# Optimization experiments

Measured on AMD Instinct MI355X. Metric: run time of the kernel, lower is better.

The kernel has to match this reference:

```python
import jax, jax.numpy as jnp
import numpy as np

CHANNELS = 32


def _mlp(x, W1, b1, W2, b2, W3, b3):
    # FNN: Linear -> ReLU -> Linear -> ReLU -> Linear (last layer linear)
    h = jax.nn.relu(x @ W1 + b1)
    h = jax.nn.relu(h @ W2 + b2)
    return h @ W3 + b3


def setup_inputs() -> dict:
    key = jax.random.key(0)
    ks = jax.random.split(key, 8)
    E = 262144
    C = CHANNELS
    H = 128
    d_in = 4  # 2 * spatial_dim
    d_out = C * (C + 1)  # 1056
    s = lambda fan_in: 1.0 / np.sqrt(fan_in)
    return {
        "pos_i": jax.random.normal(ks[0], (E, 2), jnp.float32),
        "pos_j": jax.random.normal(ks[1], (E, 2), jnp.float32),
        "v_j": jax.random.normal(ks[2], (E, C), jnp.float32),
        "W1": jax.random.normal(ks[3], (d_in, H), jnp.float32) * s(d_in),
        "b1": jnp.zeros((H,), jnp.float32),
        "W2": jax.random.normal(ks[4], (H, H), jnp.float32) * s(H),
        "b2": jnp.zeros((H,), jnp.float32),
        "W3": jax.random.normal(ks[5], (H, d_out), jnp.float32) * s(H),
        "b3": jnp.zeros((d_out,), jnp.float32),
    }


def reference(pos_i, pos_j, v_j, W1, b1, W2, b2, W3, b3):
    C = CHANNELS
    pos_ij = jnp.concatenate((pos_i, pos_j), axis=-1)          # [E, 2*spatial_dim]
    kernel = _mlp(pos_ij, W1, b1, W2, b2, W3, b3)
    kernel = kernel.reshape(-1, C, C + 1)                      # [E, C, C+1]
    mat, bias = kernel[..., :, :-1], kernel[..., :, -1]        # [E,C,C], [E,C]
    return jnp.einsum('eij,ej->ei', mat, v_j) + bias           # [E, C]
```

## Files before the change

### kernel.cpp

```cpp
#include <hip/hip_runtime.h>


#define E_TOTAL 262144
#define EPB 256
#define NBLK (E_TOTAL / EPB)

typedef float f32x4 __attribute__((ext_vector_type(4)));
typedef short s8v  __attribute__((ext_vector_type(8)));

__device__ __forceinline__ unsigned short f2bf(float x) {
  unsigned u = __float_as_uint(x);
  u += 0x7fffu + ((u >> 16) & 1u);
  return (unsigned short)(u >> 16);
}

__device__ __forceinline__ void gld16(const void* g, void* l) {
  __builtin_amdgcn_global_load_lds(
      (const __attribute__((address_space(1))) unsigned int*)g,
      (__attribute__((address_space(3))) unsigned int*)l, 16, 0, 0);
}

__global__ void prep_pack(const float* __restrict__ W2, const float* __restrict__ W3,
                          const float* __restrict__ b3,
                          unsigned short* __restrict__ Wg2, unsigned short* __restrict__ W2f,
                          unsigned short* __restrict__ b3f, float* __restrict__ b3c) {
  int idx = blockIdx.x * 256 + threadIdx.x;
  if (idx < 135168) {
    int jj = idx & 7, lane = (idx >> 3) & 63;
    int ksnn = idx >> 9, ks = ksnn & 3, nn = ksnn >> 2;
    int nnt = (nn < 33) ? (2 * nn) : (2 * (nn - 33) + 1);
    int k = ks * 32 + ((lane >> 4) << 3) + jj;
    int col = nnt * 16 + (lane & 15);
    int i = col & 31, j = col >> 5;
    Wg2[idx] = f2bf(W3[k * 1056 + i * 33 + j]);
  }
  if (idx < 16384) {
    int ks = idx >> 12, nt = (idx >> 9) & 7, l = (idx >> 3) & 63, jj = idx & 7;
    int k = ks * 32 + ((l >> 4) << 3) + jj;
    int n = nt * 16 + (l & 15);
    W2f[idx] = f2bf(W2[k * 128 + n]);
  }
  if (idx < 1024) {
    int jj = idx & 7, lane = (idx >> 3) & 63, ih = idx >> 9;
    int j = ((lane >> 4) << 3) + jj, i = ih * 16 + (lane & 15);
    b3f[idx] = f2bf(b3[i * 33 + j]);
  }
  if (idx < 32) b3c[idx] = b3[idx * 33 + 32];
}

template <int IH>
__device__ __forceinline__ void g_chunk(const unsigned short* __restrict__ buf,
                                        const float* __restrict__ vt,
                                        int j0, int lane, int eoff,
                                        const s8v (&af)[4][4], float (&oa)[2][4][4]) {
  const f32x4 zero4 = {0.f, 0.f, 0.f, 0.f};
#pragma unroll
  for (int t = 0; t < 3; ++t) {
    s8v bfr[4];
#pragma unroll
    for (int ks = 0; ks < 4; ++ks)
      bfr[ks] = *(const s8v*)&buf[t * 2048 + ks * 512 + lane * 8];
    f32x4 p[4];
#pragma unroll
    for (int m = 0; m < 4; ++m)
      p[m] = __builtin_amdgcn_mfma_f32_16x16x32_bf16(af[m][0], bfr[0], zero4, 0, 0, 0);
#pragma unroll
    for (int ks = 1; ks < 4; ++ks)
#pragma unroll
      for (int m = 0; m < 4; ++m)
        p[m] = __builtin_amdgcn_mfma_f32_16x16x32_bf16(af[m][ks], bfr[ks], p[m], 0, 0, 0);
    const float* vp = vt + (j0 + t) * 256 + eoff;
#pragma unroll
    for (int m = 0; m < 4; ++m) {
      f32x4 vv = *(const f32x4*)(vp + m * 16);
#pragma unroll
      for (int r = 0; r < 4; ++r) oa[IH][m][r] += vv[r] * p[m][r];
    }
  }
}

__global__ __launch_bounds__(256, 2) void fnn_fused(
    const float* __restrict__ pos_i, const float* __restrict__ pos_j,
    const float* __restrict__ vj, const float* __restrict__ W1,
    const float* __restrict__ b1, const float* __restrict__ b2,
    const unsigned short* __restrict__ W2f, const unsigned short* __restrict__ Wg2,
    const unsigned short* __restrict__ b3f, const float* __restrict__ b3c,
    float* __restrict__ out) {
  __shared__ __attribute__((aligned(16))) char smem[58368];
  float* vt = (float*)smem;
  unsigned short* Bb  = (unsigned short*)(smem + 33792);
  unsigned short* h1c = (unsigned short*)smem;
  unsigned short* h2n = (unsigned short*)(smem + 18432);

  const int tid = threadIdx.x;
  const int w = tid >> 6, lane = tid & 63, q = lane >> 4, ln = lane & 15;
  const int B0 = blockIdx.x * EPB;
  const int eoff = w * 64 + q * 4;

  float oa[2][4][4];
  {
    s8v av[4];
#pragma unroll
    for (int m = 0; m < 4; ++m) {
      int e = B0 + w * 64 + m * 16 + ln;
      const float4 va = *(const float4*)(vj + (size_t)e * 32 + q * 8);
      const float4 vb = *(const float4*)(vj + (size_t)e * 32 + q * 8 + 4);
      s8v t;
      t[0] = (short)f2bf(va.x); t[1] = (short)f2bf(va.y);
      t[2] = (short)f2bf(va.z); t[3] = (short)f2bf(va.w);
      t[4] = (short)f2bf(vb.x); t[5] = (short)f2bf(vb.y);
      t[6] = (short)f2bf(vb.z); t[7] = (short)f2bf(vb.w);
      av[m] = t;
    }
#pragma unroll
    for (int ih = 0; ih < 2; ++ih) {
      s8v b3fr = *(const s8v*)(b3f + (ih * 64 + lane) * 8);
      float cbv = b3c[ih * 16 + ln];
      f32x4 ci = {cbv, cbv, cbv, cbv};
#pragma unroll
      for (int m = 0; m < 4; ++m) {
        f32x4 p = __builtin_amdgcn_mfma_f32_16x16x32_bf16(av[m], b3fr, ci, 0, 0, 0);
#pragma unroll
        for (int r = 0; r < 4; ++r) oa[ih][m][r] = p[r];
      }
    }
  }

  const int hh0 = (tid & 15) * 8;
  float w1r[4][8], b1r[8], b2r[8];
#pragma unroll
  for (int d = 0; d < 4; ++d)
#pragma unroll
    for (int u = 0; u < 8; ++u) w1r[d][u] = W1[d * 128 + hh0 + u];
#pragma unroll
  for (int u = 0; u < 8; ++u) b1r[u] = b1[hh0 + u];
#pragma unroll
  for (int nt = 0; nt < 8; ++nt) b2r[nt] = b2[nt * 16 + ln];

  s8v af[4][4];
  for (int qtr = 0; qtr < 4; ++qtr) {
#pragma unroll
    for (int half = 0; half < 4; ++half) {
      int ee = (tid >> 4) + half * 16;
      int eg = B0 + qtr * 64 + ee;
      float2 pi = *(const float2*)(pos_i + (size_t)eg * 2);
      float2 pj = *(const float2*)(pos_j + (size_t)eg * 2);
      s8v hv;
#pragma unroll
      for (int u = 0; u < 8; ++u) {
        float o = b1r[u] + pi.x * w1r[0][u] + pi.y * w1r[1][u] +
                  pj.x * w1r[2][u] + pj.y * w1r[3][u];
        hv[u] = (short)f2bf(fmaxf(o, 0.f));
      }
      *(s8v*)&h1c[ee * 144 + hh0] = hv;
    }
    __syncthreads();
    {
      s8v afr[4];
#pragma unroll
      for (int ks = 0; ks < 4; ++ks)
        afr[ks] = *(const s8v*)&h1c[(w * 16 + ln) * 144 + ks * 32 + q * 8];
#pragma unroll
      for (int nt = 0; nt < 8; ++nt) {
        f32x4 a4 = {0.f, 0.f, 0.f, 0.f};
#pragma unroll
        for (int ks = 0; ks < 4; ++ks) {
          s8v bfr2 = *(const s8v*)(W2f + ((ks * 8 + nt) * 64 + lane) * 8);
          a4 = __builtin_amdgcn_mfma_f32_16x16x32_bf16(afr[ks], bfr2, a4, 0, 0, 0);
        }
#pragma unroll
        for (int r = 0; r < 4; ++r)
          h2n[(w * 16 + q * 4 + r) * 144 + nt * 16 + ln] =
              f2bf(fmaxf(a4[r] + b2r[nt], 0.f));
      }
    }
    __syncthreads();
    if (w == qtr) {
#pragma unroll
      for (int m = 0; m < 4; ++m)
#pragma unroll
        for (int ks = 0; ks < 4; ++ks)
          af[m][ks] = *(const s8v*)&h2n[(m * 16 + ln) * 144 + ks * 32 + q * 8];
    }
  }
  __syncthreads();

  {
    const float* vrow = vj + (size_t)(B0 + tid) * 32;
#pragma unroll
    for (int j4 = 0; j4 < 8; ++j4) {
      float4 vv = *(const float4*)(vrow + j4 * 4);
      vt[(j4 * 4 + 0) * 256 + tid] = vv.x;
      vt[(j4 * 4 + 1) * 256 + tid] = vv.y;
      vt[(j4 * 4 + 2) * 256 + tid] = vv.z;
      vt[(j4 * 4 + 3) * 256 + tid] = vv.w;
    }
    vt[32 * 256 + tid] = 1.0f;
  }

  {
    const char* g = (const char*)Wg2 + tid * 16;
    char* l = (char*)Bb + (tid & 192) * 16;
#pragma unroll
    for (int t = 0; t < 3; ++t) gld16(g + t * 4096, l + t * 4096);
  }
  __syncthreads();

  for (int c = 0; c < 22; ++c) {
    const unsigned short* buf = Bb + (c & 1) * 6144;
    if (c + 1 < 22) {
      const char* g = (const char*)Wg2 + (c + 1) * 12288 + tid * 16;
      char* l = (char*)Bb + ((c + 1) & 1) * 12288 + (tid & 192) * 16;
#pragma unroll
      for (int t = 0; t < 3; ++t) gld16(g + t * 4096, l + t * 4096);
    }
    if (c < 11) g_chunk<0>(buf, vt, c * 3, lane, eoff, af, oa);
    else        g_chunk<1>(buf, vt, (c - 11) * 3, lane, eoff, af, oa);
    __syncthreads();
  }

#pragma unroll
  for (int m = 0; m < 4; ++m)
#pragma unroll
    for (int ih = 0; ih < 2; ++ih)
#pragma unroll
      for (int r = 0; r < 4; ++r) {
        int e = B0 + w * 64 + m * 16 + q * 4 + r;
        out[(size_t)e * 32 + ih * 16 + ln] = oa[ih][m][r];
      }
}

extern "C" void kernel_launch(void* const* d_in, const int* in_sizes, int n_in,
                              void* d_out, int out_size, void* d_ws, size_t ws_size,
                              hipStream_t stream) {
  const float* pos_i = (const float*)d_in[0];
  const float* pos_j = (const float*)d_in[1];
  const float* vj    = (const float*)d_in[2];
  const float* W1    = (const float*)d_in[3];
  const float* b1    = (const float*)d_in[4];
  const float* W2    = (const float*)d_in[5];
  const float* b2    = (const float*)d_in[6];
  const float* W3    = (const float*)d_in[7];
  const float* b3    = (const float*)d_in[8];
  float* outp = (float*)d_out;

  unsigned short* Wg2 = (unsigned short*)d_ws;
  unsigned short* W2f = (unsigned short*)((char*)d_ws + 270336);
  unsigned short* b3f = (unsigned short*)((char*)d_ws + 303104);
  float*          b3c = (float*)((char*)d_ws + 305152);

  prep_pack<<<528, 256, 0, stream>>>(W2, W3, b3, Wg2, W2f, b3f, b3c);
  fnn_fused<<<NBLK, 256, 0, stream>>>(pos_i, pos_j, vj, W1, b1, b2, W2f, Wg2, b3f, b3c, outp);
}
```

Before: 218.9 us.

## Double edges per block to 512 and store v transpose as bf16 in LDS

Each block now handles 512 edges with 512 threads, so every W3 chunk staged in LDS is reused by twice as many edges and the per-block global-to-LDS weight traffic is amortized. The transposed v buffer is kept in bf16 to fit the larger tile in LDS, and the layer-1/2 row padding shrinks from 144 to 136. The B-fragment loads are interleaved with the MFMAs, and b2 is loaded per tile instead of held in registers to cut register pressure. In exchange, occupancy demands rise (launch bounds 512 threads with 4 blocks requested, about 68KB LDS per block), and v is rounded to bf16 in the final contraction, which lowers precision.

```diff
diff --git a/kernel.cpp b/kernel.cpp
--- a/kernel.cpp
+++ b/kernel.cpp
@@ -2,7 +2,7 @@
 
 
 #define E_TOTAL 262144
-#define EPB 256
+#define EPB 512
 #define NBLK (E_TOTAL / EPB)
 
 typedef float f32x4 __attribute__((ext_vector_type(4)));
@@ -50,47 +50,45 @@
 
 template <int IH>
 __device__ __forceinline__ void g_chunk(const unsigned short* __restrict__ buf,
-                                        const float* __restrict__ vt,
+                                        const unsigned short* __restrict__ vt,
                                         int j0, int lane, int eoff,
                                         const s8v (&af)[4][4], float (&oa)[2][4][4]) {
   const f32x4 zero4 = {0.f, 0.f, 0.f, 0.f};
 #pragma unroll
   for (int t = 0; t < 3; ++t) {
-    s8v bfr[4];
-#pragma unroll
-    for (int ks = 0; ks < 4; ++ks)
-      bfr[ks] = *(const s8v*)&buf[t * 2048 + ks * 512 + lane * 8];
+    const int j = j0 + t;
     f32x4 p[4];
 #pragma unroll
-    for (int m = 0; m < 4; ++m)
-      p[m] = __builtin_amdgcn_mfma_f32_16x16x32_bf16(af[m][0], bfr[0], zero4, 0, 0, 0);
-#pragma unroll
-    for (int ks = 1; ks < 4; ++ks)
+    for (int ks = 0; ks < 4; ++ks) {
+      s8v bfr = *(const s8v*)&buf[(t * 4 + ks) * 512 + lane * 8];
 #pragma unroll
       for (int m = 0; m < 4; ++m)
-        p[m] = __builtin_amdgcn_mfma_f32_16x16x32_bf16(af[m][ks], bfr[ks], p[m], 0, 0, 0);
-    const float* vp = vt + (j0 + t) * 256 + eoff;
+        p[m] = __builtin_amdgcn_mfma_f32_16x16x32_bf16(
+            af[m][ks], bfr, (ks == 0 ? zero4 : p[m]), 0, 0, 0);
+    }
 #pragma unroll
     for (int m = 0; m < 4; ++m) {
-      f32x4 vv = *(const f32x4*)(vp + m * 16);
-#pragma unroll
-      for (int r = 0; r < 4; ++r) oa[IH][m][r] += vv[r] * p[m][r];
-    }
-  }
-}
-
-__global__ __launch_bounds__(256, 2) void fnn_fused(
+      uint2 hv = *(const uint2*)&vt[j * 520 + eoff + m * 16];
+      oa[IH][m][0] += __uint_as_float(hv.x << 16) * p[m][0];
+      oa[IH][m][1] += __uint_as_float(hv.x & 0xffff0000u) * p[m][1];
+      oa[IH][m][2] += __uint_as_float(hv.y << 16) * p[m][2];
+      oa[IH][m][3] += __uint_as_float(hv.y & 0xffff0000u) * p[m][3];
+    }
+  }
+}
+
+__global__ __launch_bounds__(512, 4) void fnn_fused(
     const float* __restrict__ pos_i, const float* __restrict__ pos_j,
     const float* __restrict__ vj, const float* __restrict__ W1,
     const float* __restrict__ b1, const float* __restrict__ b2,
     const unsigned short* __restrict__ W2f, const unsigned short* __restrict__ Wg2,
     const unsigned short* __restrict__ b3f, const float* __restrict__ b3c,
     float* __restrict__ out) {
-  __shared__ __attribute__((aligned(16))) char smem[58368];
-  float* vt = (float*)smem;
-  unsigned short* Bb  = (unsigned short*)(smem + 33792);
+  __shared__ __attribute__((aligned(16))) char smem[69632];
+  unsigned short* vt  = (unsigned short*)smem;
   unsigned short* h1c = (unsigned short*)smem;
-  unsigned short* h2n = (unsigned short*)(smem + 18432);
+  unsigned short* h2n = (unsigned short*)(smem + 34816);
+  unsigned short* Bb  = (unsigned short*)(smem + 34816);
 
   const int tid = threadIdx.x;
   const int w = tid >> 6, lane = tid & 63, q = lane >> 4, ln = lane & 15;
@@ -127,22 +125,20 @@
   }
 
   const int hh0 = (tid & 15) * 8;
-  float w1r[4][8], b1r[8], b2r[8];
+  float w1r[4][8], b1r[8];
 #pragma unroll
   for (int d = 0; d < 4; ++d)
 #pragma unroll
     for (int u = 0; u < 8; ++u) w1r[d][u] = W1[d * 128 + hh0 + u];
 #pragma unroll
   for (int u = 0; u < 8; ++u) b1r[u] = b1[hh0 + u];
-#pragma unroll
-  for (int nt = 0; nt < 8; ++nt) b2r[nt] = b2[nt * 16 + ln];
 
   s8v af[4][4];
   for (int qtr = 0; qtr < 4; ++qtr) {
 #pragma unroll
     for (int half = 0; half < 4; ++half) {
-      int ee = (tid >> 4) + half * 16;
-      int eg = B0 + qtr * 64 + ee;
+      int ee = (tid >> 4) + half * 32;
+      int eg = B0 + qtr * 128 + ee;
       float2 pi = *(const float2*)(pos_i + (size_t)eg * 2);
       float2 pj = *(const float2*)(pos_j + (size_t)eg * 2);
       s8v hv;
@@ -152,14 +148,14 @@
                   pj.x * w1r[2][u] + pj.y * w1r[3][u];
         hv[u] = (short)f2bf(fmaxf(o, 0.f));
       }
-      *(s8v*)&h1c[ee * 144 + hh0] = hv;
+      *(s8v*)&h1c[ee * 136 + hh0] = hv;
     }
     __syncthreads();
     {
       s8v afr[4];
 #pragma unroll
       for (int ks = 0; ks < 4; ++ks)
-        afr[ks] = *(const s8v*)&h1c[(w * 16 + ln) * 144 + ks * 32 + q * 8];
+        afr[ks] = *(const s8v*)&h1c[(w * 16 + ln) * 136 + ks * 32 + q * 8];
 #pragma unroll
       for (int nt = 0; nt < 8; ++nt) {
         f32x4 a4 = {0.f, 0.f, 0.f, 0.f};
@@ -168,19 +164,20 @@
           s8v bfr2 = *(const s8v*)(W2f + ((ks * 8 + nt) * 64 + lane) * 8);
           a4 = __builtin_amdgcn_mfma_f32_16x16x32_bf16(afr[ks], bfr2, a4, 0, 0, 0);
         }
+        float b2v = b2[nt * 16 + ln];
 #pragma unroll
         for (int r = 0; r < 4; ++r)
-          h2n[(w * 16 + q * 4 + r) * 144 + nt * 16 + ln] =
-              f2bf(fmaxf(a4[r] + b2r[nt], 0.f));
+          h2n[(w * 16 + q * 4 + r) * 136 + nt * 16 + ln] =
+              f2bf(fmaxf(a4[r] + b2v, 0.f));
       }
     }
     __syncthreads();
-    if (w == qtr) {
+    if ((w >> 1) == qtr) {
 #pragma unroll
       for (int m = 0; m < 4; ++m)
 #pragma unroll
         for (int ks = 0; ks < 4; ++ks)
-          af[m][ks] = *(const s8v*)&h2n[(m * 16 + ln) * 144 + ks * 32 + q * 8];
+          af[m][ks] = *(const s8v*)&h2n[((w & 1) * 64 + m * 16 + ln) * 136 + ks * 32 + q * 8];
     }
   }
   __syncthreads();
@@ -190,29 +187,28 @@
 #pragma unroll
     for (int j4 = 0; j4 < 8; ++j4) {
       float4 vv = *(const float4*)(vrow + j4 * 4);
-      vt[(j4 * 4 + 0) * 256 + tid] = vv.x;
-      vt[(j4 * 4 + 1) * 256 + tid] = vv.y;
-      vt[(j4 * 4 + 2) * 256 + tid] = vv.z;
-      vt[(j4 * 4 + 3) * 256 + tid] = vv.w;
-    }
-    vt[32 * 256 + tid] = 1.0f;
-  }
-
-  {
-    const char* g = (const char*)Wg2 + tid * 16;
-    char* l = (char*)Bb + (tid & 192) * 16;
-#pragma unroll
-    for (int t = 0; t < 3; ++t) gld16(g + t * 4096, l + t * 4096);
-  }
+      vt[(j4 * 4 + 0) * 520 + tid] = f2bf(vv.x);
+      vt[(j4 * 4 + 1) * 520 + tid] = f2bf(vv.y);
+      vt[(j4 * 4 + 2) * 520 + tid] = f2bf(vv.z);
+      vt[(j4 * 4 + 3) * 520 + tid] = f2bf(vv.w);
+    }
+    vt[32 * 520 + tid] = 0x3F80;
+  }
+  __syncthreads();
+
+#pragma unroll 2
+  for (int u = w; u < 12; u += 8)
+    gld16((const char*)Wg2 + u * 1024 + lane * 16, (char*)Bb + u * 1024);
   __syncthreads();
 
   for (int c = 0; c < 22; ++c) {
     const unsigned short* buf = Bb + (c & 1) * 6144;
     if (c + 1 < 22) {
-      const char* g = (const char*)Wg2 + (c + 1) * 12288 + tid * 16;
-      char* l = (char*)Bb + ((c + 1) & 1) * 12288 + (tid & 192) * 16;
-#pragma unroll
-      for (int t = 0; t < 3; ++t) gld16(g + t * 4096, l + t * 4096);
+      const char* g = (const char*)Wg2 + (c + 1) * 12288;
+      char* l = (char*)Bb + ((c + 1) & 1) * 12288;
+#pragma unroll 2
+      for (int u = w; u < 12; u += 8)
+        gld16(g + u * 1024 + lane * 16, l + u * 1024);
     }
     if (c < 11) g_chunk<0>(buf, vt, c * 3, lane, eoff, af, oa);
     else        g_chunk<1>(buf, vt, (c - 11) * 3, lane, eoff, af, oa);
@@ -250,5 +246,5 @@
   float*          b3c = (float*)((char*)d_ws + 305152);
 
   prep_pack<<<528, 256, 0, stream>>>(W2, W3, b3, Wg2, W2f, b3f, b3c);
-  fnn_fused<<<NBLK, 256, 0, stream>>>(pos_i, pos_j, vj, W1, b1, b2, W2f, Wg2, b3f, b3c, outp);
-}
+  fnn_fused<<<NBLK, 512, 0, stream>>>(pos_i, pos_j, vj, W1, b1, b2, W2f, Wg2, b3f, b3c, outp);
+}
```

Result: slower. 540.9 us (+147.1%).
